# Performance work log

Measured on AMD Instinct MI355X. Metric: run time of the kernel, lower is better.

Reference implementation:

```python
import jax, jax.numpy as jnp
import numpy as np

N, E, B = 50000, 200000, 64
IN_NODE, IN_EDGE = 64, 16
D_NODE, D_EDGE, HID, L = 128, 64, 64, 6


def _w(k, shape):
    # fan-in scaled init (like torch Linear default scale)
    return jax.random.normal(k, shape, jnp.float32) / np.sqrt(shape[-2]).astype(np.float32)


def setup_inputs() -> dict:
    key = jax.random.key(0)
    ks = jax.random.split(key, 16)
    return {
        "x": jax.random.normal(ks[0], (N, IN_NODE), jnp.float32),
        "edge_attr": jax.random.normal(ks[1], (E, IN_EDGE), jnp.float32),
        "edge_index": jax.random.randint(ks[2], (2, E), 0, N),
        "batch": jnp.sort(jax.random.randint(ks[3], (N,), 0, B)),
        "lin_x_w": _w(ks[4], (IN_NODE, D_NODE)), "lin_x_b": jnp.zeros((D_NODE,), jnp.float32),
        "lin_e_w": _w(ks[5], (IN_EDGE, D_EDGE)), "lin_e_b": jnp.zeros((D_EDGE,), jnp.float32),
        "msg_w": _w(ks[6], (L, D_NODE, D_EDGE)),
        "phie_w1": _w(ks[7], (L, D_EDGE + 2 * D_NODE, HID)), "phie_b1": jnp.zeros((L, HID), jnp.float32),
        "phie_w2": _w(ks[8], (L, HID, D_EDGE)), "phie_b2": jnp.zeros((L, D_EDGE), jnp.float32),
        "phiv_w1": _w(ks[9], (L, D_NODE + D_EDGE, HID)), "phiv_b1": jnp.zeros((L, HID), jnp.float32),
        "phiv_w2": _w(ks[10], (L, HID, D_NODE)), "phiv_b2": jnp.zeros((L, D_NODE), jnp.float32),
        "ro_w1": _w(ks[11], (D_NODE, D_NODE)), "ro_b1": jnp.zeros((D_NODE,), jnp.float32),
        "ro_w2": _w(ks[12], (D_NODE, D_NODE)), "ro_b2": jnp.zeros((D_NODE,), jnp.float32),
    }


def reference(x, edge_attr, edge_index, batch,
              lin_x_w, lin_x_b, lin_e_w, lin_e_b, msg_w,
              phie_w1, phie_b1, phie_w2, phie_b2,
              phiv_w1, phiv_b1, phiv_w2, phiv_b2,
              ro_w1, ro_b1, ro_w2, ro_b2):
    src, dst = edge_index[0], edge_index[1]
    n = x.shape[0]
    h = x @ lin_x_w + lin_x_b          # [N, d_node]
    e = edge_attr @ lin_e_w + lin_e_b  # [E, d_edge]
    # per-node in-degree for scatter_mean (clamped to 1, as in torch_scatter)
    deg = jnp.maximum(jax.ops.segment_sum(jnp.ones((dst.shape[0],), h.dtype), dst, num_segments=n), 1.0)[:, None]

    def step(carry, p):
        h, e = carry
        mw, ew1, eb1, ew2, eb2, vw1, vb1, vw2, vb2 = p
        hs, hd = h[src], h[dst]                       # gathers [E, d_node]
        e_in = jnp.concatenate([hs, hd, e + hs @ mw], axis=-1)  # [E, d_edge+2*d_node]
        e = e + jax.nn.relu(e_in @ ew1 + eb1) @ ew2 + eb2
        m_dst = jax.ops.segment_sum(e, dst, num_segments=n) / deg  # scatter_mean
        v_in = jnp.concatenate([h, m_dst], axis=-1)   # [N, d_node+d_edge]
        h = h + jax.nn.relu(v_in @ vw1 + vb1) @ vw2 + vb2
        return (h, e), None

    (h, e), _ = jax.lax.scan(step, (h, e),
                             (msg_w, phie_w1, phie_b1, phie_w2, phie_b2,
                              phiv_w1, phiv_b1, phiv_w2, phiv_b2))
    # graph readout: scatter_mean over batch assignment
    gcnt = jnp.maximum(jax.ops.segment_sum(jnp.ones((n,), h.dtype), batch, num_segments=B), 1.0)[:, None]
    graph_x = jax.ops.segment_sum(h, batch, num_segments=B) / gcnt  # [B, d_node]
    return jax.nn.relu(graph_x @ ro_w1 + ro_b1) @ ro_w2 + ro_b2
```

## Files before the change

kernel.cpp:

```cpp
#include <hip/hip_runtime.h>

constexpr int Nn  = 50000;
constexpr int Ne  = 200000;
constexpr int Bg  = 64;
constexpr int DN  = 128;
constexpr int DE  = 64;
constexpr int HD  = 64;
constexpr int INN = 64;
constexpr int INE = 16;
constexpr int LAY = 6;
constexpr int SB  = 196;

typedef __attribute__((ext_vector_type(8))) short sh8;
typedef __attribute__((ext_vector_type(4))) float f4;

__device__ inline unsigned short f2bf(float x) {
  union { float f; unsigned u; } v; v.f = x;
  unsigned r = v.u + 0x7FFF + ((v.u >> 16) & 1);
  return (unsigned short)(r >> 16);
}
__device__ inline float bf2f(unsigned short u) {
  union { unsigned u; float f; } v; v.u = ((unsigned)u) << 16; return v.f;
}
__device__ inline f4 mfma16(sh8 a, sh8 b, f4 c) {
  return __builtin_amdgcn_mfma_f32_16x16x32_bf16(a, b, c, 0, 0, 0);
}

__global__ void hist(const int* __restrict__ dst, int* __restrict__ deg) {
  const int j = blockIdx.x * blockDim.x + threadIdx.x;
  if (j < Ne) atomicAdd(&deg[dst[j]], 1);
}

__global__ __launch_bounds__(256) void scan1(const int* __restrict__ deg,
                                             int* __restrict__ rp,
                                             int* __restrict__ bsum) {
  __shared__ int s[256];
  const int t = threadIdx.x, i = blockIdx.x * 256 + t;
  const int v = (i < Nn) ? deg[i] : 0;
  s[t] = v; __syncthreads();
  for (int off = 1; off < 256; off <<= 1) {
    const int x = (t >= off) ? s[t - off] : 0;
    __syncthreads();
    s[t] += x;
    __syncthreads();
  }
  if (i < Nn) rp[i] = s[t] - v;
  if (t == 255) bsum[blockIdx.x] = s[255];
}

__global__ __launch_bounds__(256) void scan2(const int* __restrict__ bsum,
                                             int* __restrict__ boff) {
  __shared__ int s[256];
  const int t = threadIdx.x;
  const int v = (t < SB) ? bsum[t] : 0;
  s[t] = v; __syncthreads();
  for (int off = 1; off < 256; off <<= 1) {
    const int x = (t >= off) ? s[t - off] : 0;
    __syncthreads();
    s[t] += x;
    __syncthreads();
  }
  if (t < SB) boff[t] = s[t] - v;
}

__global__ __launch_bounds__(256) void scan3(int* __restrict__ rp,
                                             const int* __restrict__ boff,
                                             const int* __restrict__ deg,
                                             int* __restrict__ cursor,
                                             float* __restrict__ invdeg) {
  const int i = blockIdx.x * 256 + threadIdx.x;
  if (i < Nn) {
    const int r = rp[i] + boff[i >> 8];
    rp[i] = r;
    cursor[i] = r;
    invdeg[i] = 1.0f / fmaxf((float)deg[i], 1.0f);
  }
  if (i == 0) rp[Nn] = Ne;
}

__global__ void scatter(const int* __restrict__ src, const int* __restrict__ dst,
                        int* __restrict__ cursor, int* __restrict__ pos,
                        int* __restrict__ src_s, int* __restrict__ dst_s) {
  const int j = blockIdx.x * blockDim.x + threadIdx.x;
  if (j < Ne) {
    const int d = dst[j];
    const int p = atomicAdd(&cursor[d], 1);
    pos[j] = p;
    src_s[p] = src[j];
    dst_s[p] = d;
  }
}

__global__ __launch_bounds__(64) void prep_we(const float* __restrict__ ew1,
                                              const float* __restrict__ mw,
                                              const float* __restrict__ ew2,
                                              unsigned short* __restrict__ weT,
                                              unsigned short* __restrict__ ew2T) {
  const int l = blockIdx.x >> 6, n = blockIdx.x & 63, t = threadIdx.x;
  const float* E1 = ew1 + (long)l * 320 * 64;
  const float* MW = mw + (long)l * 128 * 64;
  const float* E2 = ew2 + (long)l * 64 * 64;
  unsigned short* W = weT + (long)l * 64 * 320 + (long)n * 320;
  __shared__ float c[64];
  c[t] = E1[(256 + t) * 64 + n];
  __syncthreads();
  for (int k = t; k < 128; k += 64) {
    float s = E1[k * 64 + n];
    for (int j = 0; j < 64; ++j) s += MW[k * 64 + j] * c[j];
    W[k] = f2bf(s);
  }
  for (int k = 128 + t; k < 320; k += 64) W[k] = f2bf(E1[k * 64 + n]);
  ew2T[(long)l * 64 * 64 + n * 64 + t] = f2bf(E2[t * 64 + n]);
}

__global__ __launch_bounds__(64) void prep_wv(const float* __restrict__ vw1,
                                              const float* __restrict__ vw2,
                                              unsigned short* __restrict__ vw1T,
                                              unsigned short* __restrict__ vw2T) {
  const int l = blockIdx.x >> 7, n = blockIdx.x & 127, t = threadIdx.x;
  vw2T[(long)l * 128 * 64 + n * 64 + t] = f2bf(vw2[(long)l * 64 * 128 + t * 128 + n]);
  if (n < 64) {
    for (int k = t; k < 192; k += 64)
      vw1T[(long)l * 64 * 192 + n * 192 + k] = f2bf(vw1[(long)l * 192 * 64 + k * 64 + n]);
  }
}

__global__ __launch_bounds__(64) void prep_wx(const float* __restrict__ w,
                                              unsigned short* __restrict__ wxT) {
  const int n = blockIdx.x, t = threadIdx.x;
  wxT[n * INN + t] = f2bf(w[t * DN + n]);
}

__global__ __launch_bounds__(256) void enc_node_mfma(
    const float* __restrict__ x,
    const unsigned short* __restrict__ wxT,
    const float* __restrict__ b,
    unsigned short* __restrict__ hb) {
  const int lane = threadIdx.x & 63;
  const int wv   = threadIdx.x >> 6;
  const int quad = lane >> 4;
  const int lm   = lane & 15;
  const int wid  = blockIdx.x * 4 + wv;
  const int ntiles = (Nn + 31) / 32;
  if (wid >= ntiles) return;
  const int i0 = wid * 32;

  bool mv[2];
#pragma unroll
  for (int mt = 0; mt < 2; ++mt) mv[mt] = (i0 + mt * 16) < Nn;

  f4 acc[2][8];
#pragma unroll
  for (int mt = 0; mt < 2; ++mt)
#pragma unroll
    for (int nt = 0; nt < 8; ++nt) acc[mt][nt] = f4{0.f, 0.f, 0.f, 0.f};

#pragma unroll
  for (int ks = 0; ks < 2; ++ks) {
    const int kb = ks * 32 + quad * 8;
    sh8 a[2], bfr[8];
#pragma unroll
    for (int mt = 0; mt < 2; ++mt) {
      const int row = i0 + mt * 16 + lm;
      if (mv[mt] && row < Nn) {
        const float* xp = x + (long)row * INN + kb;
        const float4 v0 = *(const float4*)xp;
        const float4 v1 = *(const float4*)(xp + 4);
        a[mt][0] = (short)f2bf(v0.x); a[mt][1] = (short)f2bf(v0.y);
        a[mt][2] = (short)f2bf(v0.z); a[mt][3] = (short)f2bf(v0.w);
        a[mt][4] = (short)f2bf(v1.x); a[mt][5] = (short)f2bf(v1.y);
        a[mt][6] = (short)f2bf(v1.z); a[mt][7] = (short)f2bf(v1.w);
      } else a[mt] = (sh8)0;
    }
#pragma unroll
    for (int nt = 0; nt < 8; ++nt)
      bfr[nt] = *(const sh8*)(wxT + (nt * 16 + lm) * INN + kb);
#pragma unroll
    for (int mt = 0; mt < 2; ++mt)
#pragma unroll
      for (int nt = 0; nt < 8; ++nt)
        acc[mt][nt] = mfma16(a[mt], bfr[nt], acc[mt][nt]);
  }
  float bv[8];
#pragma unroll
  for (int nt = 0; nt < 8; ++nt) bv[nt] = b[nt * 16 + lm];
#pragma unroll
  for (int mt = 0; mt < 2; ++mt) {
    if (!mv[mt]) continue;
#pragma unroll
    for (int r = 0; r < 4; ++r) {
      const int row = i0 + mt * 16 + quad * 4 + r;
      if (row >= Nn) continue;
#pragma unroll
      for (int nt = 0; nt < 8; ++nt)
        hb[(long)row * DN + nt * 16 + lm] = f2bf(acc[mt][nt][r] + bv[nt]);
    }
  }
}

__global__ __launch_bounds__(256) void enc_edge(const float* __restrict__ ea,
                                                const int* __restrict__ pos,
                                                const float* __restrict__ w,
                                                const float* __restrict__ b,
                                                unsigned short* __restrict__ eb) {
  __shared__ float S[64 * INE];
  const int t = threadIdx.x;
  const int j0 = blockIdx.x * 64;
  *(float4*)&S[t * 4] = *(const float4*)&ea[(long)j0 * INE + t * 4];
  __syncthreads();
  const int lane = t & 63, wv = t >> 6;
  float wreg[INE];
#pragma unroll
  for (int k = 0; k < INE; ++k) wreg[k] = w[k * DE + lane];
  const float bias = b[lane];
#pragma unroll
  for (int el = 0; el < 16; ++el) {
    const int e = wv * 16 + el;
    float acc = bias;
#pragma unroll
    for (int k = 0; k < INE; ++k) acc += S[e * INE + k] * wreg[k];
    eb[(long)pos[j0 + e] * DE + lane] = f2bf(acc);
  }
}

constexpr int UP  = 72;
constexpr int WP1 = 328;

__global__ __launch_bounds__(256) void edge_layer_mfma(
    const unsigned short* __restrict__ hb,
    unsigned short* __restrict__ eb,
    const int* __restrict__ src_s, const int* __restrict__ dst_s,
    const unsigned short* __restrict__ weT,
    const unsigned short* __restrict__ ew2T,
    const float* __restrict__ b1, const float* __restrict__ b2) {
  __shared__ unsigned short Wl[64 * WP1];
  __shared__ unsigned short Us[4][32 * UP];
  const int t    = threadIdx.x;
  const int lane = t & 63;
  const int wv   = t >> 6;
  const int quad = lane >> 4;
  const int lm   = lane & 15;
  const int kq   = quad * 8;
  unsigned short* us = Us[wv];

#pragma unroll
  for (int c = 0; c < 10; ++c) {
    const int cc = c * 256 + t;
    const int n = cc / 40, kc = (cc % 40) * 8;
    *(sh8*)&Wl[n * WP1 + kc] = *(const sh8*)(weT + n * 320 + kc);
  }
  __syncthreads();

  float b1v[4], b2v[4];
  sh8 bi[4];
#pragma unroll
  for (int nt = 0; nt < 4; ++nt) {
    b1v[nt] = b1[nt * 16 + lm];
    b2v[nt] = b2[nt * 16 + lm];
    const int d = nt * 16 + lm - (nt >> 1) * 32 - kq;
#pragma unroll
    for (int jj = 0; jj < 8; ++jj) bi[nt][jj] = (d == jj) ? (short)0x3F80 : (short)0;
  }

  const int ntiles = Ne / 32;
  const int nw = gridDim.x * 4;
  for (int wid = blockIdx.x * 4 + wv; wid < ntiles; wid += nw) {
    const int j0 = wid * 32;

    int aoff_s[2], aoff_d[2];
#pragma unroll
    for (int mt = 0; mt < 2; ++mt) {
      const int j = j0 + mt * 16 + lm;
      aoff_s[mt] = src_s[j] * DN;
      aoff_d[mt] = dst_s[j] * DN;
    }

    sh8 a[2][10];
#pragma unroll
    for (int mt = 0; mt < 2; ++mt) {
#pragma unroll
      for (int ks = 0; ks < 4; ++ks)
        a[mt][ks] = *(const sh8*)(hb + aoff_s[mt] + ks * 32 + kq);
#pragma unroll
      for (int ks = 0; ks < 4; ++ks)
        a[mt][4 + ks] = *(const sh8*)(hb + aoff_d[mt] + ks * 32 + kq);
#pragma unroll
      for (int ks = 0; ks < 2; ++ks)
        a[mt][8 + ks] = *(const sh8*)(eb + (long)(j0 + mt * 16 + lm) * DE + ks * 32 + kq);
    }

    f4 acc[2][4];
#pragma unroll
    for (int mt = 0; mt < 2; ++mt)
#pragma unroll
      for (int nt = 0; nt < 4; ++nt) acc[mt][nt] = f4{0.f, 0.f, 0.f, 0.f};

#pragma unroll
    for (int ks = 0; ks < 10; ++ks) {
      const int kb = ks * 32 + kq;
      sh8 b[4];
#pragma unroll
      for (int nt = 0; nt < 4; ++nt)
        b[nt] = *(const sh8*)&Wl[(nt * 16 + lm) * WP1 + kb];
#pragma unroll
      for (int mt = 0; mt < 2; ++mt)
#pragma unroll
        for (int nt = 0; nt < 4; ++nt)
          acc[mt][nt] = mfma16(a[mt][ks], b[nt], acc[mt][nt]);
    }

#pragma unroll
    for (int mt = 0; mt < 2; ++mt)
#pragma unroll
      for (int nt = 0; nt < 4; ++nt)
#pragma unroll
        for (int r = 0; r < 4; ++r) {
          const int row = mt * 16 + quad * 4 + r;
          const int col = nt * 16 + lm;
          us[row * UP + col] = f2bf(fmaxf(acc[mt][nt][r] + b1v[nt], 0.f));
        }

    f4 acc2[2][4];
#pragma unroll
    for (int mt = 0; mt < 2; ++mt)
#pragma unroll
      for (int nt = 0; nt < 4; ++nt) acc2[mt][nt] = f4{0.f, 0.f, 0.f, 0.f};
#pragma unroll
    for (int ks = 0; ks < 2; ++ks) {
      const int kb = ks * 32 + kq;
      sh8 au[2], b[4];
#pragma unroll
      for (int mt = 0; mt < 2; ++mt)
        au[mt] = *(const sh8*)&us[(mt * 16 + lm) * UP + kb];
#pragma unroll
      for (int nt = 0; nt < 4; ++nt)
        b[nt] = *(const sh8*)(ew2T + (nt * 16 + lm) * 64 + kb);
#pragma unroll
      for (int mt = 0; mt < 2; ++mt)
#pragma unroll
        for (int nt = 0; nt < 4; ++nt)
          acc2[mt][nt] = mfma16(au[mt], b[nt], acc2[mt][nt]);
    }
#pragma unroll
    for (int nt = 0; nt < 4; ++nt)
#pragma unroll
      for (int mt = 0; mt < 2; ++mt)
        acc2[mt][nt] = mfma16(a[mt][8 + (nt >> 1)], bi[nt], acc2[mt][nt]);

#pragma unroll
    for (int mt = 0; mt < 2; ++mt)
#pragma unroll
      for (int nt = 0; nt < 4; ++nt)
#pragma unroll
        for (int r = 0; r < 4; ++r)
          us[(mt * 16 + quad * 4 + r) * UP + nt * 16 + lm] =
              f2bf(acc2[mt][nt][r] + b2v[nt]);
#pragma unroll
    for (int s = 0; s < 4; ++s) {
      const int row = s * 8 + (lane >> 3);
      const sh8 v = *(const sh8*)&us[row * UP + (lane & 7) * 8];
      *(sh8*)(eb + (long)(j0 + row) * DE + (lane & 7) * 8) = v;
    }
  }
}

constexpr int VP1 = 200;
constexpr int VP2 = 72;
constexpr int V2OFF = 64 * VP1;

__global__ __launch_bounds__(256) void node_layer_mfma(
    unsigned short* __restrict__ hb,
    const unsigned short* __restrict__ eb,
    const int* __restrict__ rp,
    const float* __restrict__ invdeg,
    const unsigned short* __restrict__ vw1T,
    const unsigned short* __restrict__ vw2T,
    const float* __restrict__ b1, const float* __restrict__ b2) {
  __shared__ unsigned short Wl[64 * VP1 + 128 * VP2];
  __shared__ unsigned short Us[4][32 * UP];
  const int t    = threadIdx.x;
  const int lane = t & 63;
  const int wv   = t >> 6;
  const int quad = lane >> 4;
  const int lm   = lane & 15;
  const int kq   = quad * 8;
  unsigned short* us = Us[wv];

#pragma unroll
  for (int c = 0; c < 6; ++c) {
    const int cc = c * 256 + t;
    const int n = cc / 24, kc = (cc % 24) * 8;
    *(sh8*)&Wl[n * VP1 + kc] = *(const sh8*)(vw1T + n * 192 + kc);
  }
#pragma unroll
  for (int c = 0; c < 4; ++c) {
    const int cc = c * 256 + t;
    const int n = cc / 8, kc = (cc % 8) * 8;
    *(sh8*)&Wl[V2OFF + n * VP2 + kc] = *(const sh8*)(vw2T + n * 64 + kc);
  }
  __syncthreads();

  float b1v[4];
  sh8 bi[4];
#pragma unroll
  for (int nt = 0; nt < 4; ++nt) {
    b1v[nt] = b1[nt * 16 + lm];
    const int d = nt * 16 + lm - (nt >> 1) * 32 - kq;
#pragma unroll
    for (int jj = 0; jj < 8; ++jj) bi[nt][jj] = (d == jj) ? (short)0x3F80 : (short)0;
  }
  float b2v[2][4];
#pragma unroll
  for (int nh = 0; nh < 2; ++nh)
#pragma unroll
    for (int nt = 0; nt < 4; ++nt) b2v[nh][nt] = b2[nh * 64 + nt * 16 + lm];

  const int ntiles = (Nn + 31) / 32;
  const int nw = gridDim.x * 4;
  for (int wid = blockIdx.x * 4 + wv; wid < ntiles; wid += nw) {
    const int i0 = wid * 32;
    bool mv[2];
#pragma unroll
    for (int mt = 0; mt < 2; ++mt) mv[mt] = (i0 + mt * 16) < Nn;

    sh8 a[2][6];
#pragma unroll
    for (int mt = 0; mt < 2; ++mt) {
      const int row = i0 + mt * 16 + lm;
      if (mv[mt]) {
#pragma unroll
        for (int ks = 0; ks < 4; ++ks)
          a[mt][ks] = *(const sh8*)(hb + (long)row * DN + ks * 32 + kq);
        const int js = rp[row], je = rp[row + 1];
        float m0[8], m1[8];
#pragma unroll
        for (int c = 0; c < 8; ++c) { m0[c] = 0.f; m1[c] = 0.f; }
        for (int j = js; j < je; ++j) {
          const sh8 v0 = *(const sh8*)(eb + (long)j * DE + kq);
          const sh8 v1 = *(const sh8*)(eb + (long)j * DE + 32 + kq);
#pragma unroll
          for (int c = 0; c < 8; ++c) {
            m0[c] += bf2f((unsigned short)v0[c]);
            m1[c] += bf2f((unsigned short)v1[c]);
          }
        }
        const float inv = invdeg[row];
        sh8 f0, f1;
#pragma unroll
        for (int c = 0; c < 8; ++c) {
          f0[c] = (short)f2bf(m0[c] * inv);
          f1[c] = (short)f2bf(m1[c] * inv);
        }
        a[mt][4] = f0;
        a[mt][5] = f1;
      } else {
#pragma unroll
        for (int ks = 0; ks < 6; ++ks) a[mt][ks] = (sh8)0;
      }
    }

    f4 acc[2][4];
#pragma unroll
    for (int mt = 0; mt < 2; ++mt)
#pragma unroll
      for (int nt = 0; nt < 4; ++nt) acc[mt][nt] = f4{0.f, 0.f, 0.f, 0.f};
#pragma unroll
    for (int ks = 0; ks < 6; ++ks) {
      const int kb = ks * 32 + kq;
      sh8 b[4];
#pragma unroll
      for (int nt = 0; nt < 4; ++nt)
        b[nt] = *(const sh8*)&Wl[(nt * 16 + lm) * VP1 + kb];
#pragma unroll
      for (int mt = 0; mt < 2; ++mt)
#pragma unroll
        for (int nt = 0; nt < 4; ++nt)
          acc[mt][nt] = mfma16(a[mt][ks], b[nt], acc[mt][nt]);
    }
#pragma unroll
    for (int mt = 0; mt < 2; ++mt)
#pragma unroll
      for (int nt = 0; nt < 4; ++nt)
#pragma unroll
        for (int r = 0; r < 4; ++r) {
          const int row = mt * 16 + quad * 4 + r;
          const int col = nt * 16 + lm;
          us[row * UP + col] = f2bf(fmaxf(acc[mt][nt][r] + b1v[nt], 0.f));
        }

    sh8 au[2][2];
#pragma unroll
    for (int ks = 0; ks < 2; ++ks)
#pragma unroll
      for (int mt = 0; mt < 2; ++mt)
        au[mt][ks] = *(const sh8*)&us[(mt * 16 + lm) * UP + ks * 32 + kq];

#pragma unroll
    for (int nh = 0; nh < 2; ++nh) {
      f4 acc2[2][4];
#pragma unroll
      for (int mt = 0; mt < 2; ++mt)
#pragma unroll
        for (int nt = 0; nt < 4; ++nt) acc2[mt][nt] = f4{0.f, 0.f, 0.f, 0.f};
#pragma unroll
      for (int ks = 0; ks < 2; ++ks) {
        const int kb = ks * 32 + kq;
        sh8 b[4];
#pragma unroll
        for (int nt = 0; nt < 4; ++nt)
          b[nt] = *(const sh8*)&Wl[V2OFF + (nh * 64 + nt * 16 + lm) * VP2 + kb];
#pragma unroll
        for (int mt = 0; mt < 2; ++mt)
#pragma unroll
          for (int nt = 0; nt < 4; ++nt)
            acc2[mt][nt] = mfma16(au[mt][ks], b[nt], acc2[mt][nt]);
      }
#pragma unroll
      for (int nt = 0; nt < 4; ++nt)
#pragma unroll
        for (int mt = 0; mt < 2; ++mt)
          acc2[mt][nt] = mfma16(a[mt][nh * 2 + (nt >> 1)], bi[nt], acc2[mt][nt]);

#pragma unroll
      for (int mt = 0; mt < 2; ++mt)
#pragma unroll
        for (int nt = 0; nt < 4; ++nt)
#pragma unroll
          for (int r = 0; r < 4; ++r)
            us[(mt * 16 + quad * 4 + r) * UP + nt * 16 + lm] =
                f2bf(acc2[mt][nt][r] + b2v[nh][nt]);
#pragma unroll
      for (int s = 0; s < 4; ++s) {
        const int row = s * 8 + (lane >> 3);
        if (i0 + row < Nn) {
          const sh8 v = *(const sh8*)&us[row * UP + (lane & 7) * 8];
          *(sh8*)(hb + (long)(i0 + row) * DN + nh * 64 + (lane & 7) * 8) = v;
        }
      }
    }
  }
}

constexpr int GB = 512;

__global__ __launch_bounds__(128) void graph_acc(const unsigned short* __restrict__ hb,
                                                 const int* __restrict__ batch,
                                                 float* __restrict__ gacc,
                                                 float* __restrict__ gcnt) {
  const int c = threadIdx.x;
  const int per = (Nn + GB - 1) / GB;
  const int s0 = blockIdx.x * per;
  const int s1 = min(s0 + per, Nn);
  if (s0 >= s1) return;
  int cur = batch[s0];
  float acc = 0.f, cnt = 0.f;
  for (int i = s0; i < s1; ++i) {
    const int b = batch[i];
    if (b != cur) {
      atomicAdd(&gacc[cur * DN + c], acc);
      if (c == 0) atomicAdd(&gcnt[cur], cnt);
      acc = 0.f; cnt = 0.f; cur = b;
    }
    acc += bf2f(hb[(long)i * DN + c]);
    cnt += 1.f;
  }
  atomicAdd(&gacc[cur * DN + c], acc);
  if (c == 0) atomicAdd(&gcnt[cur], cnt);
}

__global__ __launch_bounds__(128) void readout(const float* __restrict__ gacc,
                                               const float* __restrict__ gcnt,
                                               const float* __restrict__ w1,
                                               const float* __restrict__ b1,
                                               const float* __restrict__ w2,
                                               const float* __restrict__ b2,
                                               float* __restrict__ out) {
  __shared__ float g[DN], t1[DN];
  const int b = blockIdx.x, c = threadIdx.x;
  const float inv = 1.0f / fmaxf(gcnt[b], 1.0f);
  g[c] = gacc[b * DN + c] * inv;
  __syncthreads();
  float acc = b1[c];
  for (int k = 0; k < DN; ++k) acc += g[k] * w1[k * DN + c];
  t1[c] = fmaxf(acc, 0.0f);
  __syncthreads();
  acc = b2[c];
  for (int k = 0; k < DN; ++k) acc += t1[k] * w2[k * DN + c];
  out[b * DN + c] = acc;
}

extern "C" void kernel_launch(void* const* d_in, const int* in_sizes, int n_in,
                              void* d_out, int out_size, void* d_ws, size_t ws_size,
                              hipStream_t stream) {
  const float* x       = (const float*)d_in[0];
  const float* ea      = (const float*)d_in[1];
  const int*   ei      = (const int*)d_in[2];
  const int*   batch   = (const int*)d_in[3];
  const float* lin_x_w = (const float*)d_in[4];
  const float* lin_x_b = (const float*)d_in[5];
  const float* lin_e_w = (const float*)d_in[6];
  const float* lin_e_b = (const float*)d_in[7];
  const float* msg_w   = (const float*)d_in[8];
  const float* phie_w1 = (const float*)d_in[9];
  const float* phie_b1 = (const float*)d_in[10];
  const float* phie_w2 = (const float*)d_in[11];
  const float* phie_b2 = (const float*)d_in[12];
  const float* phiv_w1 = (const float*)d_in[13];
  const float* phiv_b1 = (const float*)d_in[14];
  const float* phiv_w2 = (const float*)d_in[15];
  const float* phiv_b2 = (const float*)d_in[16];
  const float* ro_w1   = (const float*)d_in[17];
  const float* ro_b1   = (const float*)d_in[18];
  const float* ro_w2   = (const float*)d_in[19];
  const float* ro_b2   = (const float*)d_in[20];

  const int* srcp = ei;
  const int* dstp = ei + Ne;

  int*   deg_i  = (int*)d_ws;
  float* gacc   = (float*)(deg_i + Nn);
  float* gcnt   = gacc + Bg * DN;
  float* invdeg = gcnt + Bg;
  int*   row_ptr= (int*)(invdeg + Nn);
  int*   cursor = row_ptr + Nn + 8;
  int*   bsum   = cursor + Nn;
  int*   boff   = bsum + 256;
  int*   pos    = boff + 256;
  int*   src_s  = pos + Ne;
  int*   dst_s  = src_s + Ne;
  unsigned short* hb   = (unsigned short*)(dst_s + Ne);
  unsigned short* eb   = hb + (long)Nn * DN;
  unsigned short* weT  = eb + (long)Ne * DE;
  unsigned short* ew2T = weT + (long)LAY * 64 * 320;
  unsigned short* vw1T = ew2T + (long)LAY * 64 * 64;
  unsigned short* vw2T = vw1T + (long)LAY * 64 * 192;
  unsigned short* wxT  = vw2T + (long)LAY * 128 * 64;

  hipMemsetAsync(deg_i, 0, sizeof(int) * Nn + sizeof(float) * (Bg * DN + Bg), stream);

  hist<<<(Ne + 255) / 256, 256, 0, stream>>>(dstp, deg_i);
  scan1<<<SB, 256, 0, stream>>>(deg_i, row_ptr, bsum);
  scan2<<<1, 256, 0, stream>>>(bsum, boff);
  scan3<<<SB, 256, 0, stream>>>(row_ptr, boff, deg_i, cursor, invdeg);
  scatter<<<(Ne + 255) / 256, 256, 0, stream>>>(srcp, dstp, cursor, pos, src_s, dst_s);

  prep_we<<<LAY * 64, 64, 0, stream>>>(phie_w1, msg_w, phie_w2, weT, ew2T);
  prep_wv<<<LAY * 128, 64, 0, stream>>>(phiv_w1, phiv_w2, vw1T, vw2T);
  prep_wx<<<DN, 64, 0, stream>>>(lin_x_w, wxT);

  const int encblocks = ((Nn + 31) / 32 + 3) / 4;
  enc_node_mfma<<<encblocks, 256, 0, stream>>>(x, wxT, lin_x_b, hb);
  enc_edge<<<Ne / 64, 256, 0, stream>>>(ea, pos, lin_e_w, lin_e_b, eb);

  const int eblocks = 512;
  const int vblocks = 512;

  for (int l = 0; l < LAY; ++l) {
    edge_layer_mfma<<<eblocks, 256, 0, stream>>>(
        hb, eb, src_s, dst_s,
        weT + (long)l * 64 * 320, ew2T + (long)l * 64 * 64,
        phie_b1 + (long)l * HD, phie_b2 + (long)l * DE);
    node_layer_mfma<<<vblocks, 256, 0, stream>>>(
        hb, eb, row_ptr, invdeg,
        vw1T + (long)l * 64 * 192, vw2T + (long)l * 128 * 64,
        phiv_b1 + (long)l * HD, phiv_b2 + (long)l * DN);
  }

  graph_acc<<<GB, 128, 0, stream>>>(hb, batch, gacc, gcnt);
  readout<<<Bg, 128, 0, stream>>>(gacc, gcnt, ro_w1, ro_b1, ro_w2, ro_b2,
                                  (float*)d_out);
}
```

Baseline: 625.5 us.

## Precompute per-node projections of h before edge MLP instead of per-edge

```diff
diff --git a/kernel.cpp b/kernel.cpp
--- a/kernel.cpp
+++ b/kernel.cpp
@@ -94,22 +94,24 @@
 __global__ __launch_bounds__(64) void prep_we(const float* __restrict__ ew1,
                                               const float* __restrict__ mw,
                                               const float* __restrict__ ew2,
-                                              unsigned short* __restrict__ weT,
+                                              unsigned short* __restrict__ wpT,
+                                              unsigned short* __restrict__ w1eT,
                                               unsigned short* __restrict__ ew2T) {
   const int l = blockIdx.x >> 6, n = blockIdx.x & 63, t = threadIdx.x;
   const float* E1 = ew1 + (long)l * 320 * 64;
   const float* MW = mw + (long)l * 128 * 64;
   const float* E2 = ew2 + (long)l * 64 * 64;
-  unsigned short* W = weT + (long)l * 64 * 320 + (long)n * 320;
+  unsigned short* WP = wpT + (long)l * 128 * 128;
   __shared__ float c[64];
   c[t] = E1[(256 + t) * 64 + n];
   __syncthreads();
   for (int k = t; k < 128; k += 64) {
     float s = E1[k * 64 + n];
     for (int j = 0; j < 64; ++j) s += MW[k * 64 + j] * c[j];
-    W[k] = f2bf(s);
-  }
-  for (int k = 128 + t; k < 320; k += 64) W[k] = f2bf(E1[k * 64 + n]);
+    WP[n * 128 + k] = f2bf(s);
+    WP[(64 + n) * 128 + k] = f2bf(E1[(128 + k) * 64 + n]);
+  }
+  w1eT[(long)l * 64 * 64 + n * 64 + t] = f2bf(E1[(256 + t) * 64 + n]);
   ew2T[(long)l * 64 * 64 + n * 64 + t] = f2bf(E2[t * 64 + n]);
 }
 
@@ -223,17 +225,91 @@
   }
 }
 
-constexpr int UP  = 72;
-constexpr int WP1 = 328;
+constexpr int PP = 136;
+
+__global__ __launch_bounds__(256) void proj_mfma(
+    const unsigned short* __restrict__ hb,
+    const unsigned short* __restrict__ wpT,
+    unsigned short* __restrict__ P) {
+  __shared__ unsigned short Us[4][32 * PP];
+  const int lane = threadIdx.x & 63;
+  const int wv   = threadIdx.x >> 6;
+  const int quad = lane >> 4;
+  const int lm   = lane & 15;
+  const int kq   = quad * 8;
+  const int wid  = blockIdx.x * 4 + wv;
+  const int ntiles = (Nn + 31) / 32;
+  if (wid >= ntiles) return;
+  const int i0 = wid * 32;
+  unsigned short* us = Us[wv];
+
+  bool mv[2];
+#pragma unroll
+  for (int mt = 0; mt < 2; ++mt) mv[mt] = (i0 + mt * 16) < Nn;
+
+  sh8 a[2][4];
+#pragma unroll
+  for (int mt = 0; mt < 2; ++mt) {
+    const int row = i0 + mt * 16 + lm;
+    if (mv[mt]) {
+#pragma unroll
+      for (int ks = 0; ks < 4; ++ks)
+        a[mt][ks] = *(const sh8*)(hb + (long)row * DN + ks * 32 + kq);
+    } else {
+#pragma unroll
+      for (int ks = 0; ks < 4; ++ks) a[mt][ks] = (sh8)0;
+    }
+  }
+
+  f4 acc[2][8];
+#pragma unroll
+  for (int mt = 0; mt < 2; ++mt)
+#pragma unroll
+    for (int nt = 0; nt < 8; ++nt) acc[mt][nt] = f4{0.f, 0.f, 0.f, 0.f};
+
+#pragma unroll
+  for (int ks = 0; ks < 4; ++ks) {
+    const int kb = ks * 32 + kq;
+    sh8 bfr[8];
+#pragma unroll
+    for (int nt = 0; nt < 8; ++nt)
+      bfr[nt] = *(const sh8*)(wpT + (nt * 16 + lm) * 128 + kb);
+#pragma unroll
+    for (int mt = 0; mt < 2; ++mt)
+#pragma unroll
+      for (int nt = 0; nt < 8; ++nt)
+        acc[mt][nt] = mfma16(a[mt][ks], bfr[nt], acc[mt][nt]);
+  }
+
+#pragma unroll
+  for (int mt = 0; mt < 2; ++mt)
+#pragma unroll
+    for (int nt = 0; nt < 8; ++nt)
+#pragma unroll
+      for (int r = 0; r < 4; ++r)
+        us[(mt * 16 + quad * 4 + r) * PP + nt * 16 + lm] = f2bf(acc[mt][nt][r]);
+#pragma unroll
+  for (int s = 0; s < 8; ++s) {
+    const int row = s * 4 + (lane >> 4);
+    const int col8 = (lane & 15) * 8;
+    if (i0 + row < Nn) {
+      const sh8 v = *(const sh8*)&us[row * PP + col8];
+      *(sh8*)(P + (long)(i0 + row) * 128 + col8) = v;
+    }
+  }
+}
+
+constexpr int UP = 72;
 
 __global__ __launch_bounds__(256) void edge_layer_mfma(
-    const unsigned short* __restrict__ hb,
+    const unsigned short* __restrict__ P,
     unsigned short* __restrict__ eb,
     const int* __restrict__ src_s, const int* __restrict__ dst_s,
-    const unsigned short* __restrict__ weT,
+    const unsigned short* __restrict__ w1eT,
     const unsigned short* __restrict__ ew2T,
     const float* __restrict__ b1, const float* __restrict__ b2) {
-  __shared__ unsigned short Wl[64 * WP1];
+  __shared__ unsigned short W1l[64 * UP];
+  __shared__ unsigned short W2l[64 * UP];
   __shared__ unsigned short Us[4][32 * UP];
   const int t    = threadIdx.x;
   const int lane = t & 63;
@@ -244,10 +320,11 @@
   unsigned short* us = Us[wv];
 
 #pragma unroll
-  for (int c = 0; c < 10; ++c) {
+  for (int c = 0; c < 2; ++c) {
     const int cc = c * 256 + t;
-    const int n = cc / 40, kc = (cc % 40) * 8;
-    *(sh8*)&Wl[n * WP1 + kc] = *(const sh8*)(weT + n * 320 + kc);
+    const int n = cc >> 3, kc = (cc & 7) * 8;
+    *(sh8*)&W1l[n * UP + kc] = *(const sh8*)(w1eT + n * 64 + kc);
+    *(sh8*)&W2l[n * UP + kc] = *(const sh8*)(ew2T + n * 64 + kc);
   }
   __syncthreads();
 
@@ -267,26 +344,18 @@
   for (int wid = blockIdx.x * 4 + wv; wid < ntiles; wid += nw) {
     const int j0 = wid * 32;
 
-    int aoff_s[2], aoff_d[2];
+    sh8 as_[2][2], ad_[2][2], ae_[2][2];
 #pragma unroll
     for (int mt = 0; mt < 2; ++mt) {
       const int j = j0 + mt * 16 + lm;
-      aoff_s[mt] = src_s[j] * DN;
-      aoff_d[mt] = dst_s[j] * DN;
-    }
-
-    sh8 a[2][10];
-#pragma unroll
-    for (int mt = 0; mt < 2; ++mt) {
-#pragma unroll
-      for (int ks = 0; ks < 4; ++ks)
-        a[mt][ks] = *(const sh8*)(hb + aoff_s[mt] + ks * 32 + kq);
-#pragma unroll
-      for (int ks = 0; ks < 4; ++ks)
-        a[mt][4 + ks] = *(const sh8*)(hb + aoff_d[mt] + ks * 32 + kq);
-#pragma unroll
-      for (int ks = 0; ks < 2; ++ks)
-        a[mt][8 + ks] = *(const sh8*)(eb + (long)(j0 + mt * 16 + lm) * DE + ks * 32 + kq);
+      const long srow = (long)src_s[j] * 128;
+      const long drow = (long)dst_s[j] * 128 + 64;
+#pragma unroll
+      for (int ks = 0; ks < 2; ++ks) {
+        as_[mt][ks] = *(const sh8*)(P + srow + ks * 32 + kq);
+        ad_[mt][ks] = *(const sh8*)(P + drow + ks * 32 + kq);
+        ae_[mt][ks] = *(const sh8*)(eb + (long)j * DE + ks * 32 + kq);
+      }
     }
 
     f4 acc[2][4];
@@ -294,20 +363,26 @@
     for (int mt = 0; mt < 2; ++mt)
 #pragma unroll
       for (int nt = 0; nt < 4; ++nt) acc[mt][nt] = f4{0.f, 0.f, 0.f, 0.f};
-
-#pragma unroll
-    for (int ks = 0; ks < 10; ++ks) {
+#pragma unroll
+    for (int ks = 0; ks < 2; ++ks) {
       const int kb = ks * 32 + kq;
       sh8 b[4];
 #pragma unroll
       for (int nt = 0; nt < 4; ++nt)
-        b[nt] = *(const sh8*)&Wl[(nt * 16 + lm) * WP1 + kb];
+        b[nt] = *(const sh8*)&W1l[(nt * 16 + lm) * UP + kb];
 #pragma unroll
       for (int mt = 0; mt < 2; ++mt)
 #pragma unroll
         for (int nt = 0; nt < 4; ++nt)
-          acc[mt][nt] = mfma16(a[mt][ks], b[nt], acc[mt][nt]);
-    }
+          acc[mt][nt] = mfma16(ae_[mt][ks], b[nt], acc[mt][nt]);
+    }
+#pragma unroll
+    for (int nt = 0; nt < 4; ++nt)
+#pragma unroll
+      for (int mt = 0; mt < 2; ++mt) {
+        acc[mt][nt] = mfma16(as_[mt][nt >> 1], bi[nt], acc[mt][nt]);
+        acc[mt][nt] = mfma16(ad_[mt][nt >> 1], bi[nt], acc[mt][nt]);
+      }
 
 #pragma unroll
     for (int mt = 0; mt < 2; ++mt)
@@ -334,7 +409,7 @@
         au[mt] = *(const sh8*)&us[(mt * 16 + lm) * UP + kb];
 #pragma unroll
       for (int nt = 0; nt < 4; ++nt)
-        b[nt] = *(const sh8*)(ew2T + (nt * 16 + lm) * 64 + kb);
+        b[nt] = *(const sh8*)&W2l[(nt * 16 + lm) * UP + kb];
 #pragma unroll
       for (int mt = 0; mt < 2; ++mt)
 #pragma unroll
@@ -345,7 +420,7 @@
     for (int nt = 0; nt < 4; ++nt)
 #pragma unroll
       for (int mt = 0; mt < 2; ++mt)
-        acc2[mt][nt] = mfma16(a[mt][8 + (nt >> 1)], bi[nt], acc2[mt][nt]);
+        acc2[mt][nt] = mfma16(ae_[mt][nt >> 1], bi[nt], acc2[mt][nt]);
 
 #pragma unroll
     for (int mt = 0; mt < 2; ++mt)
@@ -630,8 +705,10 @@
   int*   dst_s  = src_s + Ne;
   unsigned short* hb   = (unsigned short*)(dst_s + Ne);
   unsigned short* eb   = hb + (long)Nn * DN;
-  unsigned short* weT  = eb + (long)Ne * DE;
-  unsigned short* ew2T = weT + (long)LAY * 64 * 320;
+  unsigned short* Pm   = eb + (long)Ne * DE;
+  unsigned short* wpT  = Pm + (long)Nn * 128;
+  unsigned short* w1eT = wpT + (long)LAY * 128 * 128;
+  unsigned short* ew2T = w1eT + (long)LAY * 64 * 64;
   unsigned short* vw1T = ew2T + (long)LAY * 64 * 64;
   unsigned short* vw2T = vw1T + (long)LAY * 64 * 192;
   unsigned short* wxT  = vw2T + (long)LAY * 128 * 64;
@@ -644,21 +721,22 @@
   scan3<<<SB, 256, 0, stream>>>(row_ptr, boff, deg_i, cursor, invdeg);
   scatter<<<(Ne + 255) / 256, 256, 0, stream>>>(srcp, dstp, cursor, pos, src_s, dst_s);
 
-  prep_we<<<LAY * 64, 64, 0, stream>>>(phie_w1, msg_w, phie_w2, weT, ew2T);
+  prep_we<<<LAY * 64, 64, 0, stream>>>(phie_w1, msg_w, phie_w2, wpT, w1eT, ew2T);
   prep_wv<<<LAY * 128, 64, 0, stream>>>(phiv_w1, phiv_w2, vw1T, vw2T);
   prep_wx<<<DN, 64, 0, stream>>>(lin_x_w, wxT);
 
-  const int encblocks = ((Nn + 31) / 32 + 3) / 4;
-  enc_node_mfma<<<encblocks, 256, 0, stream>>>(x, wxT, lin_x_b, hb);
+  const int tblocks = ((Nn + 31) / 32 + 3) / 4;
+  enc_node_mfma<<<tblocks, 256, 0, stream>>>(x, wxT, lin_x_b, hb);
   enc_edge<<<Ne / 64, 256, 0, stream>>>(ea, pos, lin_e_w, lin_e_b, eb);
 
-  const int eblocks = 512;
+  const int eblocks = 1024;
   const int vblocks = 512;
 
   for (int l = 0; l < LAY; ++l) {
+    proj_mfma<<<tblocks, 256, 0, stream>>>(hb, wpT + (long)l * 128 * 128, Pm);
     edge_layer_mfma<<<eblocks, 256, 0, stream>>>(
-        hb, eb, src_s, dst_s,
-        weT + (long)l * 64 * 320, ew2T + (long)l * 64 * 64,
+        Pm, eb, src_s, dst_s,
+        w1eT + (long)l * 64 * 64, ew2T + (long)l * 64 * 64,
         phie_b1 + (long)l * HD, phie_b2 + (long)l * DE);
     node_layer_mfma<<<vblocks, 256, 0, stream>>>(
         hb, eb, row_ptr, invdeg,
```

Measured after the change: 518.0 us, median of 2. 17.2% less time.
